# Performance work log

Measured on AMD Instinct MI355X. Metric: run time of the kernel, lower is better.

## Reference

```python
import jax, jax.numpy as jnp
import numpy as np

N_NODES = 200000
D_IN = 512
HID = 512
D_OUT = 256
B = 1024
SIZES = (25, 10)


def setup_inputs() -> dict:
    key = jax.random.key(0)
    ks = jax.random.split(key, 8)
    x = jax.random.normal(ks[0], (N_NODES, D_IN), dtype=jnp.float32)
    nodes = jax.random.randint(ks[1], (B,), 0, N_NODES)
    neigh1 = jax.random.randint(ks[2], (B * SIZES[0],), 0, N_NODES)
    neigh2 = jax.random.randint(ks[3], (B * SIZES[0] * SIZES[1],), 0, N_NODES)
    # SAGEAggregator weights, stored as [in, out] (torch Linear weight transposed); bias=False
    s = 0.05
    Ws0 = jax.random.normal(ks[4], (D_IN, HID), dtype=jnp.float32) * s
    Wn0 = jax.random.normal(ks[5], (D_IN, HID), dtype=jnp.float32) * s
    Ws1 = jax.random.normal(ks[6], (2 * HID, D_OUT), dtype=jnp.float32) * s
    Wn1 = jax.random.normal(ks[7], (2 * HID, D_OUT), dtype=jnp.float32) * s
    return {"x": x, "nodes": nodes, "neigh1": neigh1, "neigh2": neigh2,
            "Ws0": Ws0, "Wn0": Wn0, "Ws1": Ws1, "Wn1": Wn1}


def _sage_agg(h_self, h_neigh, Ws, Wn, concat):
    # h_self: [M, d], h_neigh: [M, fanout, d] -> mean aggregate then linear transforms
    m = jnp.mean(h_neigh, axis=1)
    a = h_self @ Ws
    b = m @ Wn
    return jnp.concatenate([a, b], axis=-1) if concat else a + b


def reference(x, nodes, neigh1, neigh2, Ws0, Wn0, Ws1, Wn1):
    # gather features for root nodes and sampled 1-hop / 2-hop neighborhoods
    h0 = x[nodes]    # [B, D_IN]
    h1 = x[neigh1]   # [B*25, D_IN]
    h2 = x[neigh2]   # [B*25*10, D_IN]
    d = D_IN
    # layer 0 (concat=True), act=relu, dropout is identity (inference)
    h0 = jax.nn.relu(_sage_agg(h0, h1.reshape(-1, SIZES[0], d), Ws0, Wn0, True))  # [B, 2*HID]
    h1 = jax.nn.relu(_sage_agg(h1, h2.reshape(-1, SIZES[1], d), Ws0, Wn0, True))  # [B*25, 2*HID]
    d2 = 2 * HID
    # layer 1 (last aggregator, concat=False -> sum), no activation
    out = _sage_agg(h0, h1.reshape(-1, SIZES[0], d2), Ws1, Wn1, False)  # [B, D_OUT]
    return out
```

## Files before the change

kernel.cpp:

```cpp
#include <hip/hip_runtime.h>
#include <hip/hip_bf16.h>


#define DEVINL __device__ __forceinline__

typedef __bf16 bf16x8 __attribute__((ext_vector_type(8)));
typedef float f32x4 __attribute__((ext_vector_type(4)));

DEVINL unsigned short f2bf(float f) {
  union { float f; unsigned u; } v; v.f = f;
  unsigned r = v.u + 0x7FFFu + ((v.u >> 16) & 1u);
  return (unsigned short)(r >> 16);
}
DEVINL float bf2f(unsigned short h) {
  union { unsigned u; float f; } v; v.u = ((unsigned)h) << 16;
  return v.f;
}

DEVINL void gload_lds16(const void* g, void* l) {
  __builtin_amdgcn_global_load_lds(
      (const __attribute__((address_space(1))) void*)g,
      (__attribute__((address_space(3))) void*)l, 16, 0, 0);
}

template <int EPI>
DEVINL void gemm_core(const unsigned short* __restrict__ A, int lda,
                      const unsigned short* __restrict__ Bt, int ldb,
                      int Kc, long tm, long tn, int col0,
                      unsigned short* __restrict__ C1, float* __restrict__ out, int ldc,
                      unsigned short* As, unsigned short* Bs) {
  const int t = threadIdx.x;
  const int w = t >> 6;
  const int l = t & 63;
  const int wm = w >> 1, wn = w & 1;
  f32x4 acc[4][4] = {};
  const int s_r = l >> 2;
  const int s_kc = (l & 3) * 8;

  for (int kt = 0; kt < Kc; kt += 32) {
    __syncthreads();
    #pragma unroll
    for (int r = 0; r < 2; ++r) {
      const int chunk = r * 64 + w * 16;
      gload_lds16(A + (size_t)(tm + chunk + s_r) * lda + kt + s_kc, As + chunk * 32);
      gload_lds16(Bt + (size_t)(tn + chunk + s_r) * ldb + kt + s_kc, Bs + chunk * 32);
    }
    __syncthreads();

    bf16x8 af[4], bfr[4];
    const unsigned short* Ab = As + ((size_t)(wm * 64 + (l & 15)) * 32 + (l >> 4) * 8);
    const unsigned short* Bb = Bs + ((size_t)(wn * 64 + (l & 15)) * 32 + (l >> 4) * 8);
    #pragma unroll
    for (int f = 0; f < 4; ++f) {
      af[f] = *reinterpret_cast<const bf16x8*>(Ab + f * 16 * 32);
      bfr[f] = *reinterpret_cast<const bf16x8*>(Bb + f * 16 * 32);
    }
    #pragma unroll
    for (int i = 0; i < 4; ++i)
      #pragma unroll
      for (int j = 0; j < 4; ++j)
        acc[i][j] = __builtin_amdgcn_mfma_f32_16x16x32_bf16(af[i], bfr[j], acc[i][j], 0, 0, 0);
  }

  const int q = l >> 4, cl = l & 15;
  #pragma unroll
  for (int i = 0; i < 4; ++i)
    #pragma unroll
    for (int j = 0; j < 4; ++j)
      #pragma unroll
      for (int r = 0; r < 4; ++r) {
        const long row = tm + wm * 64 + i * 16 + q * 4 + r;
        const long col = col0 + tn + wn * 64 + j * 16 + cl;
        if (EPI == 0) C1[row * 1024 + col] = f2bf(fmaxf(acc[i][j][r], 0.f));
        else          atomicAdd(out + row * ldc + col, acc[i][j][r]);
      }
}

__global__ __launch_bounds__(256) void phase0_kernel(
    const float* __restrict__ x, const int* __restrict__ neigh1, const int* __restrict__ nodes,
    const float* __restrict__ Ws0, const float* __restrict__ Wn0,
    const float* __restrict__ Ws1, const float* __restrict__ Wn1,
    unsigned short* __restrict__ Hall,
    unsigned short* __restrict__ WT0s, unsigned short* __restrict__ WT0n,
    unsigned short* __restrict__ WT1s, unsigned short* __restrict__ WT1n,
    float* __restrict__ out) {
  const int b = blockIdx.x;
  const int tid = threadIdx.x;
  if (b < 13312) {
    int row = b * 2 + (tid >> 7);
    int src = row < 25600 ? neigh1[row] : nodes[row - 25600];
    int c4 = (tid & 127) << 2;
    const float4 v = *reinterpret_cast<const float4*>(x + (size_t)src * 512 + c4);
    ushort4 o; o.x = f2bf(v.x); o.y = f2bf(v.y); o.z = f2bf(v.z); o.w = f2bf(v.w);
    *reinterpret_cast<ushort4*>(Hall + (size_t)row * 512 + c4) = o;
  } else if (b < 13312 + 4096) {
    int t = (b - 13312) * 256 + tid;
    int region = t >> 18, local = t & 262143;
    const float* W; unsigned short* WT;
    if (region == 0)      { W = Ws0; WT = WT0s; }
    else if (region == 1) { W = Wn0; WT = WT0n; }
    else if (region == 2) { W = Ws1; WT = WT1s; }
    else                  { W = Wn1; WT = WT1n; }
    int k, n, N;
    if (region < 2) { k = local & 511;  n = local >> 9;  N = 512; }
    else            { k = local & 1023; n = local >> 10; N = 256; }
    WT[local] = f2bf(W[(size_t)k * N + n]);
  } else {
    int t = (b - 17408) * 256 + tid;
    reinterpret_cast<float4*>(out)[t] = float4{0.f, 0.f, 0.f, 0.f};
  }
}

__global__ __launch_bounds__(256) void phase1_kernel(
    const float* __restrict__ x, const int* __restrict__ neigh2,
    const unsigned short* __restrict__ Hall, const unsigned short* __restrict__ WT0s,
    unsigned short* __restrict__ Hmall, unsigned short* __restrict__ C1all) {
  __shared__ __align__(16) unsigned short As[128 * 32];
  __shared__ __align__(16) unsigned short Bs[128 * 32];
  const int b = blockIdx.x;
  const int tid = threadIdx.x;
  if (b < 832) {
    const long tm = (long)(b >> 2) * 128;
    const long tn = (long)(b & 3) * 128;
    gemm_core<0>(Hall, 512, WT0s, 512, 512, tm, tn, 0, C1all, nullptr, 0, As, Bs);
  } else if (b < 832 + 12800) {
    int row = (b - 832) * 2 + (tid >> 7);
    int c4 = (tid & 127) << 2;
    float4 acc = {0.f, 0.f, 0.f, 0.f};
    const int* ip = neigh2 + (size_t)row * 10;
    #pragma unroll
    for (int j = 0; j < 10; ++j) {
      const float4 v = *reinterpret_cast<const float4*>(x + (size_t)ip[j] * 512 + c4);
      acc.x += v.x; acc.y += v.y; acc.z += v.z; acc.w += v.w;
    }
    const float s = 0.1f;
    ushort4 o; o.x = f2bf(acc.x * s); o.y = f2bf(acc.y * s);
    o.z = f2bf(acc.z * s); o.w = f2bf(acc.w * s);
    *reinterpret_cast<ushort4*>(Hmall + (size_t)row * 512 + c4) = o;
  } else {
    int g = (b - 13632) * 2 + (tid >> 7);
    int c4 = (tid & 127) << 2;
    float a0 = 0, a1 = 0, a2 = 0, a3 = 0;
    for (int j = 0; j < 25; ++j) {
      ushort4 v = *reinterpret_cast<const ushort4*>(Hall + ((size_t)g * 25 + j) * 512 + c4);
      a0 += bf2f(v.x); a1 += bf2f(v.y); a2 += bf2f(v.z); a3 += bf2f(v.w);
    }
    const float s = 1.0f / 25.0f;
    ushort4 o; o.x = f2bf(a0 * s); o.y = f2bf(a1 * s); o.z = f2bf(a2 * s); o.w = f2bf(a3 * s);
    *reinterpret_cast<ushort4*>(Hmall + ((size_t)25600 + g) * 512 + c4) = o;
  }
}

__global__ __launch_bounds__(256) void phase2_kernel(
    const unsigned short* __restrict__ Hmall, const unsigned short* __restrict__ WT0n,
    unsigned short* __restrict__ C1all) {
  __shared__ __align__(16) unsigned short As[128 * 32];
  __shared__ __align__(16) unsigned short Bs[128 * 32];
  const long tm = (long)(blockIdx.x >> 2) * 128;
  const long tn = (long)(blockIdx.x & 3) * 128;
  gemm_core<0>(Hmall, 512, WT0n, 512, 512, tm, tn, 512, C1all, nullptr, 0, As, Bs);
}

__global__ __launch_bounds__(256) void phase3_kernel(const unsigned short* __restrict__ C1all,
                                                     unsigned short* __restrict__ M1) {
  int g = blockIdx.x;
  int c4 = threadIdx.x << 2;
  float a0 = 0, a1 = 0, a2 = 0, a3 = 0;
  for (int j = 0; j < 25; ++j) {
    ushort4 v = *reinterpret_cast<const ushort4*>(C1all + ((size_t)g * 25 + j) * 1024 + c4);
    a0 += bf2f(v.x); a1 += bf2f(v.y); a2 += bf2f(v.z); a3 += bf2f(v.w);
  }
  const float s = 1.0f / 25.0f;
  ushort4 o; o.x = f2bf(a0 * s); o.y = f2bf(a1 * s); o.z = f2bf(a2 * s); o.w = f2bf(a3 * s);
  *reinterpret_cast<ushort4*>(M1 + (size_t)g * 1024 + c4) = o;
}

__global__ __launch_bounds__(256) void gemm1_kernel(
    const unsigned short* __restrict__ C0, const unsigned short* __restrict__ WT1s,
    const unsigned short* __restrict__ M1, const unsigned short* __restrict__ WT1n,
    float* __restrict__ out) {
  __shared__ __align__(16) unsigned short As[128 * 32];
  __shared__ __align__(16) unsigned short Bs[128 * 32];
  const int pass = blockIdx.z >> 2;
  const int k0 = (blockIdx.z & 3) * 256;
  gemm_core<1>((pass ? M1 : C0) + k0, 1024, (pass ? WT1n : WT1s) + k0, 1024, 256,
               (long)blockIdx.y * 128, (long)blockIdx.x * 128, 0,
               nullptr, out, 256, As, Bs);
}

extern "C" void kernel_launch(void* const* d_in, const int* in_sizes, int n_in,
                              void* d_out, int out_size, void* d_ws, size_t ws_size,
                              hipStream_t stream) {
  const float* x      = (const float*)d_in[0];
  const int*   nodes  = (const int*)d_in[1];
  const int*   neigh1 = (const int*)d_in[2];
  const int*   neigh2 = (const int*)d_in[3];
  const float* Ws0    = (const float*)d_in[4];
  const float* Wn0    = (const float*)d_in[5];
  const float* Ws1    = (const float*)d_in[6];
  const float* Wn1    = (const float*)d_in[7];
  float* out = (float*)d_out;

  char* p = (char*)d_ws;
  unsigned short* WT0s  = (unsigned short*)p; p += (size_t)512 * 512 * 2;
  unsigned short* WT0n  = (unsigned short*)p; p += (size_t)512 * 512 * 2;
  unsigned short* WT1s  = (unsigned short*)p; p += (size_t)256 * 1024 * 2;
  unsigned short* WT1n  = (unsigned short*)p; p += (size_t)256 * 1024 * 2;
  unsigned short* Hall  = (unsigned short*)p; p += (size_t)26624 * 512 * 2;
  unsigned short* Hmall = (unsigned short*)p; p += (size_t)26624 * 512 * 2;
  unsigned short* C1all = (unsigned short*)p; p += (size_t)26624 * 1024 * 2;
  unsigned short* M1    = (unsigned short*)p; p += (size_t)1024 * 1024 * 2;

  const unsigned short* C0 = C1all + (size_t)25600 * 1024;

  hipLaunchKernelGGL(phase0_kernel, dim3(17664), dim3(256), 0, stream,
                     x, neigh1, nodes, Ws0, Wn0, Ws1, Wn1,
                     Hall, WT0s, WT0n, WT1s, WT1n, out);
  hipLaunchKernelGGL(phase1_kernel, dim3(14144), dim3(256), 0, stream,
                     x, neigh2, Hall, WT0s, Hmall, C1all);
  hipLaunchKernelGGL(phase2_kernel, dim3(832), dim3(256), 0, stream,
                     Hmall, WT0n, C1all);
  hipLaunchKernelGGL(phase3_kernel, dim3(1024), dim3(256), 0, stream, C1all, M1);
  hipLaunchKernelGGL(gemm1_kernel, dim3(2, 8, 8), dim3(256), 0, stream,
                     C0, WT1s, M1, WT1n, out);
}
```

Measured before the change: 177.6 us.

## Overlap neighbor mean reductions with GEMMs and widen K tile to 64

```diff
diff --git a/kernel.cpp b/kernel.cpp
--- a/kernel.cpp
+++ b/kernel.cpp
@@ -23,7 +23,7 @@
       (__attribute__((address_space(3))) void*)l, 16, 0, 0);
 }
 
-template <int EPI>
+template <int EPI, int BK>
 DEVINL void gemm_core(const unsigned short* __restrict__ A, int lda,
                       const unsigned short* __restrict__ Bt, int ldb,
                       int Kc, long tm, long tn, int col0,
@@ -34,32 +34,40 @@
   const int l = t & 63;
   const int wm = w >> 1, wn = w & 1;
   f32x4 acc[4][4] = {};
-  const int s_r = l >> 2;
-  const int s_kc = (l & 3) * 8;
-
-  for (int kt = 0; kt < Kc; kt += 32) {
+  constexpr int LPR = BK / 8;
+  constexpr int RPW = 64 / LPR;
+  constexpr int ROUNDS = 128 / (4 * RPW);
+  constexpr int NS = BK / 32;
+  const int s_r = l / LPR;
+  const int s_kc = (l % LPR) * 8;
+
+  for (int kt = 0; kt < Kc; kt += BK) {
     __syncthreads();
     #pragma unroll
-    for (int r = 0; r < 2; ++r) {
-      const int chunk = r * 64 + w * 16;
-      gload_lds16(A + (size_t)(tm + chunk + s_r) * lda + kt + s_kc, As + chunk * 32);
-      gload_lds16(Bt + (size_t)(tn + chunk + s_r) * ldb + kt + s_kc, Bs + chunk * 32);
+    for (int r = 0; r < ROUNDS; ++r) {
+      const int chunk = r * (4 * RPW) + w * RPW;
+      gload_lds16(A + (size_t)(tm + chunk + s_r) * lda + kt + s_kc, As + chunk * BK);
+      gload_lds16(Bt + (size_t)(tn + chunk + s_r) * ldb + kt + s_kc, Bs + chunk * BK);
     }
     __syncthreads();
 
-    bf16x8 af[4], bfr[4];
-    const unsigned short* Ab = As + ((size_t)(wm * 64 + (l & 15)) * 32 + (l >> 4) * 8);
-    const unsigned short* Bb = Bs + ((size_t)(wn * 64 + (l & 15)) * 32 + (l >> 4) * 8);
-    #pragma unroll
-    for (int f = 0; f < 4; ++f) {
-      af[f] = *reinterpret_cast<const bf16x8*>(Ab + f * 16 * 32);
-      bfr[f] = *reinterpret_cast<const bf16x8*>(Bb + f * 16 * 32);
-    }
-    #pragma unroll
-    for (int i = 0; i < 4; ++i)
+    bf16x8 af[4][NS], bfr[4][NS];
+    const unsigned short* Ab = As + ((size_t)(wm * 64 + (l & 15)) * BK + (l >> 4) * 8);
+    const unsigned short* Bb = Bs + ((size_t)(wn * 64 + (l & 15)) * BK + (l >> 4) * 8);
+    #pragma unroll
+    for (int f = 0; f < 4; ++f)
       #pragma unroll
-      for (int j = 0; j < 4; ++j)
-        acc[i][j] = __builtin_amdgcn_mfma_f32_16x16x32_bf16(af[i], bfr[j], acc[i][j], 0, 0, 0);
+      for (int s = 0; s < NS; ++s) {
+        af[f][s] = *reinterpret_cast<const bf16x8*>(Ab + f * 16 * BK + s * 32);
+        bfr[f][s] = *reinterpret_cast<const bf16x8*>(Bb + f * 16 * BK + s * 32);
+      }
+    #pragma unroll
+    for (int s = 0; s < NS; ++s)
+      #pragma unroll
+      for (int i = 0; i < 4; ++i)
+        #pragma unroll
+        for (int j = 0; j < 4; ++j)
+          acc[i][j] = __builtin_amdgcn_mfma_f32_16x16x32_bf16(af[i][s], bfr[j][s], acc[i][j], 0, 0, 0);
   }
 
   const int q = l >> 4, cl = l & 15;
@@ -74,6 +82,18 @@
         if (EPI == 0) C1[row * 1024 + col] = f2bf(fmaxf(acc[i][j][r], 0.f));
         else          atomicAdd(out + row * ldc + col, acc[i][j][r]);
       }
+}
+
+DEVINL void mean25_c1(const unsigned short* __restrict__ C1all,
+                      unsigned short* __restrict__ M1, int g, int c) {
+  float a0 = 0, a1 = 0, a2 = 0, a3 = 0;
+  for (int j = 0; j < 25; ++j) {
+    ushort4 v = *reinterpret_cast<const ushort4*>(C1all + ((size_t)g * 25 + j) * 1024 + c);
+    a0 += bf2f(v.x); a1 += bf2f(v.y); a2 += bf2f(v.z); a3 += bf2f(v.w);
+  }
+  const float s = 1.0f / 25.0f;
+  ushort4 o; o.x = f2bf(a0 * s); o.y = f2bf(a1 * s); o.z = f2bf(a2 * s); o.w = f2bf(a3 * s);
+  *reinterpret_cast<ushort4*>(M1 + (size_t)g * 1024 + c) = o;
 }
 
 __global__ __launch_bounds__(256) void phase0_kernel(
@@ -122,7 +142,7 @@
   if (b < 832) {
     const long tm = (long)(b >> 2) * 128;
     const long tn = (long)(b & 3) * 128;
-    gemm_core<0>(Hall, 512, WT0s, 512, 512, tm, tn, 0, C1all, nullptr, 0, As, Bs);
+    gemm_core<0, 32>(Hall, 512, WT0s, 512, 512, tm, tn, 0, C1all, nullptr, 0, As, Bs);
   } else if (b < 832 + 12800) {
     int row = (b - 832) * 2 + (tid >> 7);
     int c4 = (tid & 127) << 2;
@@ -153,39 +173,54 @@
 
 __global__ __launch_bounds__(256) void phase2_kernel(
     const unsigned short* __restrict__ Hmall, const unsigned short* __restrict__ WT0n,
-    unsigned short* __restrict__ C1all) {
-  __shared__ __align__(16) unsigned short As[128 * 32];
-  __shared__ __align__(16) unsigned short Bs[128 * 32];
-  const long tm = (long)(blockIdx.x >> 2) * 128;
-  const long tn = (long)(blockIdx.x & 3) * 128;
-  gemm_core<0>(Hmall, 512, WT0n, 512, 512, tm, tn, 512, C1all, nullptr, 0, As, Bs);
-}
-
-__global__ __launch_bounds__(256) void phase3_kernel(const unsigned short* __restrict__ C1all,
-                                                     unsigned short* __restrict__ M1) {
-  int g = blockIdx.x;
-  int c4 = threadIdx.x << 2;
-  float a0 = 0, a1 = 0, a2 = 0, a3 = 0;
-  for (int j = 0; j < 25; ++j) {
-    ushort4 v = *reinterpret_cast<const ushort4*>(C1all + ((size_t)g * 25 + j) * 1024 + c4);
-    a0 += bf2f(v.x); a1 += bf2f(v.y); a2 += bf2f(v.z); a3 += bf2f(v.w);
-  }
-  const float s = 1.0f / 25.0f;
-  ushort4 o; o.x = f2bf(a0 * s); o.y = f2bf(a1 * s); o.z = f2bf(a2 * s); o.w = f2bf(a3 * s);
-  *reinterpret_cast<ushort4*>(M1 + (size_t)g * 1024 + c4) = o;
-}
-
-__global__ __launch_bounds__(256) void gemm1_kernel(
+    unsigned short* __restrict__ C1all, unsigned short* __restrict__ M1) {
+  __shared__ __align__(16) unsigned short As[128 * 64];
+  __shared__ __align__(16) unsigned short Bs[128 * 64];
+  const int b = blockIdx.x;
+  if (b < 832) {
+    const long tm = (long)(b >> 2) * 128;
+    const long tn = (long)(b & 3) * 128;
+    gemm_core<0, 64>(Hmall, 512, WT0n, 512, 512, tm, tn, 512, C1all, nullptr, 0, As, Bs);
+  } else {
+    int g = (b - 832) * 2 + (threadIdx.x >> 7);
+    int c = (threadIdx.x & 127) << 2;
+    mean25_c1(C1all, M1, g, c);
+  }
+}
+
+__global__ __launch_bounds__(256) void phase4_kernel(
     const unsigned short* __restrict__ C0, const unsigned short* __restrict__ WT1s,
     const unsigned short* __restrict__ M1, const unsigned short* __restrict__ WT1n,
+    const unsigned short* __restrict__ C1all, unsigned short* __restrict__ M1w,
     float* __restrict__ out) {
-  __shared__ __align__(16) unsigned short As[128 * 32];
-  __shared__ __align__(16) unsigned short Bs[128 * 32];
-  const int pass = blockIdx.z >> 2;
-  const int k0 = (blockIdx.z & 3) * 256;
-  gemm_core<1>((pass ? M1 : C0) + k0, 1024, (pass ? WT1n : WT1s) + k0, 1024, 256,
-               (long)blockIdx.y * 128, (long)blockIdx.x * 128, 0,
-               nullptr, out, 256, As, Bs);
+  __shared__ __align__(16) unsigned short As[128 * 64];
+  __shared__ __align__(16) unsigned short Bs[128 * 64];
+  const int b = blockIdx.x;
+  if (b < 64) {
+    const int z = b >> 4, bm = (b >> 1) & 7, bn = b & 1;
+    gemm_core<1, 64>(C0 + z * 256, 1024, WT1s + z * 256, 1024, 256,
+                     (long)bm * 128, (long)bn * 128, 0, nullptr, out, 256, As, Bs);
+  } else if (b < 96) {
+    const int zz = b - 64;
+    const int z = zz >> 4, bm = (zz >> 1) & 7, bn = zz & 1;
+    gemm_core<1, 64>(M1 + z * 256, 1024, WT1n + z * 256, 1024, 256,
+                     (long)bm * 128, (long)bn * 128, 0, nullptr, out, 256, As, Bs);
+  } else {
+    int g = (b - 96) * 2 + (threadIdx.x >> 7);
+    int c = 512 + ((threadIdx.x & 127) << 2);
+    mean25_c1(C1all, M1w, g, c);
+  }
+}
+
+__global__ __launch_bounds__(256) void phase5_kernel(
+    const unsigned short* __restrict__ M1, const unsigned short* __restrict__ WT1n,
+    float* __restrict__ out) {
+  __shared__ __align__(16) unsigned short As[128 * 64];
+  __shared__ __align__(16) unsigned short Bs[128 * 64];
+  const int b = blockIdx.x;
+  const int z = 2 + (b >> 4), bm = (b >> 1) & 7, bn = b & 1;
+  gemm_core<1, 64>(M1 + z * 256, 1024, WT1n + z * 256, 1024, 256,
+                   (long)bm * 128, (long)bn * 128, 0, nullptr, out, 256, As, Bs);
 }
 
 extern "C" void kernel_launch(void* const* d_in, const int* in_sizes, int n_in,
@@ -218,9 +253,10 @@
                      Hall, WT0s, WT0n, WT1s, WT1n, out);
   hipLaunchKernelGGL(phase1_kernel, dim3(14144), dim3(256), 0, stream,
                      x, neigh2, Hall, WT0s, Hmall, C1all);
-  hipLaunchKernelGGL(phase2_kernel, dim3(832), dim3(256), 0, stream,
-                     Hmall, WT0n, C1all);
-  hipLaunchKernelGGL(phase3_kernel, dim3(1024), dim3(256), 0, stream, C1all, M1);
-  hipLaunchKernelGGL(gemm1_kernel, dim3(2, 8, 8), dim3(256), 0, stream,
-                     C0, WT1s, M1, WT1n, out);
-}
+  hipLaunchKernelGGL(phase2_kernel, dim3(1344), dim3(256), 0, stream,
+                     Hmall, WT0n, C1all, M1);
+  hipLaunchKernelGGL(phase4_kernel, dim3(608), dim3(256), 0, stream,
+                     C0, WT1s, M1, WT1n, C1all, M1, out);
+  hipLaunchKernelGGL(phase5_kernel, dim3(32), dim3(256), 0, stream,
+                     M1, WT1n, out);
+}
```

New measurement: 178.8 us. About the same (+0.7%).
